# Performance work log

Measured on AMD Instinct MI355X. Metric: run time of the kernel, lower is better.

Reference implementation:

```python
import jax, jax.numpy as jnp
import numpy as np

T, B, D, H, A = 512, 1024, 128, 64, 18


def _mlp(x, W1, b1, W2, b2):
    # two Linear+ReLU layers (MLP with hidden_sizes=(64,64), output_dim=0)
    h = jax.nn.relu(x @ W1.T + b1)
    return jax.nn.relu(h @ W2.T + b2)


def _gru_scan(x, dones, h0, Wih, Whh, bih, bhh):
    # x: [T,B,H], dones: [T,B], h0: [1,B,H]; torch GRU cell with done-reset
    def step(h, inp):
        xt, dt = inp
        h = (1.0 - dt)[:, None] * h  # reset state where episode ended
        gi = xt @ Wih.T + bih        # [B,3H]
        gh = h @ Whh.T + bhh
        ir, iz, i_n = jnp.split(gi, 3, axis=-1)
        hr, hz, h_n = jnp.split(gh, 3, axis=-1)
        r = jax.nn.sigmoid(ir + hr)
        z = jax.nn.sigmoid(iz + hz)
        n = jnp.tanh(i_n + r * h_n)
        h_new = (1.0 - z) * n + z * h
        return h_new, h_new
    hT, hs = jax.lax.scan(step, h0[0], (x, dones))
    return hs, hT[None]  # [T,B,H], [1,B,H]


def setup_inputs() -> dict:
    key = jax.random.key(0)
    ks = jax.random.split(key, 24)
    u = lambda k, shape, fan_in: jax.random.uniform(k, shape, jnp.float32, -1.0, 1.0) / np.sqrt(fan_in)
    inp = {
        'obs': jax.random.normal(ks[0], (T, B, D), jnp.float32),
        'dones': (jax.random.uniform(ks[1], (T, B)) < 0.01).astype(jnp.float32),
        'actor_state': jnp.zeros((1, B, H), jnp.float32),
        'critic_state': jnp.zeros((1, B, H), jnp.float32),
        # actor params
        'aW1': u(ks[2], (H, D), D), 'ab1': u(ks[3], (H,), D),
        'aW2': u(ks[4], (H, H), H), 'ab2': u(ks[5], (H,), H),
        'aWih': u(ks[6], (3 * H, H), H), 'aWhh': u(ks[7], (3 * H, H), H),
        'abih': u(ks[8], (3 * H,), H), 'abhh': u(ks[9], (3 * H,), H),
        'aWl': u(ks[10], (A, H), H), 'abl': u(ks[11], (A,), H),
        # critic params
        'cW1': u(ks[12], (H, D), D), 'cb1': u(ks[13], (H,), D),
        'cW2': u(ks[14], (H, H), H), 'cb2': u(ks[15], (H,), H),
        'cWih': u(ks[16], (3 * H, H), H), 'cWhh': u(ks[17], (3 * H, H), H),
        'cbih': u(ks[18], (3 * H,), H), 'cbhh': u(ks[19], (3 * H,), H),
        'cWv': u(ks[20], (1, H), H), 'cbv': u(ks[21], (1,), H),
    }
    return inp


def reference(obs, dones, actor_state, critic_state,
              aW1, ab1, aW2, ab2, aWih, aWhh, abih, abhh, aWl, abl,
              cW1, cb1, cW2, cb2, cWih, cWhh, cbih, cbhh, cWv, cbv):
    # actor branch
    xa = _mlp(obs, aW1, ab1, aW2, ab2)                              # [T,B,H]
    ha, actor_state = _gru_scan(xa, dones, actor_state, aWih, aWhh, abih, abhh)
    logits = ha @ aWl.T + abl                                       # [T,B,A]
    # critic branch
    xc = _mlp(obs, cW1, cb1, cW2, cb2)
    hc, critic_state = _gru_scan(xc, dones, critic_state, cWih, cWhh, cbih, cbhh)
    values = hc @ cWv.T + cbv                                       # [T,B,1]
    return (logits, values, actor_state, critic_state)
```

## Files before the change

### kernel.cpp

```cpp
#include <hip/hip_runtime.h>
#include <hip/hip_bf16.h>

typedef short short8 __attribute__((ext_vector_type(8)));
typedef float f32x4 __attribute__((ext_vector_type(4)));

#define T_ 512
#define B_ 1024
#define D_ 128
#define H_ 64
#define A_ 18
#define TB_ (T_*B_)

#define XELEMS (TB_*H_)
#define WBASE  (2*XELEMS)
#define WBR    38912
#define W1OFF  0
#define W2OFF  8192
#define WIHOFF 12288
#define WHHOFF 24576
#define WHDOFF 36864

#define LOGN  (TB_*A_)
#define VOFF_ LOGN
#define SOFF_ (LOGN + TB_)

#define S1_ (-1.4426950408889634f)
#define S2_ (-2.885390081777927f)

__device__ __forceinline__ ushort f2bf(float f) {
  __hip_bfloat16 h = __float2bfloat16(f);
  return __builtin_bit_cast(ushort, h);
}
__device__ __forceinline__ uint cvt_pk_bf16(float lo, float hi) {
  uint r;
  asm("v_cvt_pk_bf16_f32 %0, %1, %2" : "=v"(r) : "v"(lo), "v"(hi));
  return r;
}
__device__ __forceinline__ ushort cvt1_bf16(float v) {
  return (ushort)(cvt_pk_bf16(v, v) & 0xffffu);
}
__device__ __forceinline__ f32x4 mfma16(short8 a, short8 b, f32x4 c) {
  return __builtin_amdgcn_mfma_f32_16x16x32_bf16(a, b, c, 0, 0, 0);
}

__global__ __launch_bounds__(256) void prep_kernel(
    const float* aW1, const float* aW2, const float* aWih, const float* aWhh, const float* aWl,
    const float* cW1, const float* cW2, const float* cWih, const float* cWhh, const float* cWv,
    ushort* wts) {
  int idx = blockIdx.x * 256 + threadIdx.x;
  if (idx >= 2*WBR) return;
  int br = idx / WBR, off = idx % WBR;
  float v;
  if      (off < W2OFF)  v = (br ? cW1  : aW1 )[off];
  else if (off < WIHOFF) v = (br ? cW2  : aW2 )[off - W2OFF];
  else if (off < WHHOFF) {
    int rel = off - WIHOFF;
    v = (br ? cWih : aWih)[rel];
    v *= (rel < 128*H_) ? S1_ : S2_;
  }
  else if (off < WHDOFF) {
    int rel = off - WHHOFF;
    v = (br ? cWhh : aWhh)[rel];
    v *= (rel < 128*H_) ? S1_ : S2_;
  }
  else {
    int t = off - WHDOFF;
    if (br == 0) v = (t < A_*H_) ? aWl[t] : 0.f;
    else         v = (t < H_)    ? cWv[t] : 0.f;
  }
  wts[WBASE + idx] = f2bf(v);
}

__global__ __launch_bounds__(256) void mlp_kernel(
    const float* __restrict__ obs, const ushort* __restrict__ wts,
    const float* __restrict__ ab1, const float* __restrict__ ab2,
    const float* __restrict__ cb1, const float* __restrict__ cb2,
    ushort* __restrict__ xout) {
  __shared__ __align__(16) ushort htA[4][16 * H_], htC[4][16 * H_];
  __shared__ __align__(16) ushort wlds[24576];
  const int tid = threadIdx.x;
  const int l = tid & 63, w = tid >> 6;
  const int lr = l & 15, lg = l >> 4;
  const int key = lr & 7;
  const long base = (long)blockIdx.x * 256;
  const ushort* wbA = wts + WBASE;
  const ushort* wbC = wts + WBASE + WBR;

  float b1A[4], b1C[4], b2A[4], b2C[4];
  #pragma unroll
  for (int nt = 0; nt < 4; ++nt) {
    int coln = nt * 16 + lr;
    b1A[nt] = ab1[coln]; b1C[nt] = cb1[coln];
    b2A[nt] = ab2[coln]; b2C[nt] = cb2[coln];
  }

  #pragma unroll
  for (int i = 0; i < 12; ++i) {
    int c = tid + i * 256;
    int seg = (c < 1024) ? 0 : (c < 2048) ? 1 : (c < 2560) ? 2 : 3;
    int cbase = (seg == 0) ? 0 : (seg == 1) ? 1024 : (seg == 2) ? 2048 : 2560;
    int off = (c - cbase) * 8;
    int L = (seg < 2) ? 128 : 64;
    int segdst = (seg == 0) ? 0 : (seg == 1) ? 8192 : (seg == 2) ? 16384 : 20480;
    const ushort* src = (seg == 0) ? wbA + W1OFF + off :
                        (seg == 1) ? wbC + W1OFF + off :
                        (seg == 2) ? wbA + W2OFF + off : wbC + W2OFF + off;
    int n = off / L, ci = (off % L) / 8;
    int cis = (ci & ~7) | ((ci & 7) ^ (n & 7));
    *(uint4*)(wlds + segdst + n * L + cis * 8) = *(const uint4*)src;
  }
  __syncthreads();

  auto getW1 = [&](int br, int n, int ks) -> short8 {
    int ci = ks * 4 + lg;
    int cis = (ci & 8) | ((ci & 7) ^ (n & 7));
    return *(const short8*)(wlds + br * 8192 + n * D_ + cis * 8);
  };
  auto getW2 = [&](int br, int n, int ks) -> short8 {
    int ci = ks * 4 + lg;
    int cis = ci ^ (n & 7);
    return *(const short8*)(wlds + 16384 + br * 4096 + n * H_ + cis * 8);
  };

  auto ldobs = [&](int s, float4 (&buf)[8]) {
    const float* op = obs + (base + s * 64 + (long)w * 16 + lr) * D_;
    #pragma unroll
    for (int ks = 0; ks < 4; ++ks) {
      buf[2 * ks]     = *(const float4*)(op + ks * 32 + lg * 8);
      buf[2 * ks + 1] = *(const float4*)(op + ks * 32 + lg * 8 + 4);
    }
  };

  auto compute = [&](int s, float4 (&buf)[8]) {
    short8 af[4];
    #pragma unroll
    for (int ks = 0; ks < 4; ++ks) {
      uint4 u;
      u.x = cvt_pk_bf16(buf[2 * ks].x, buf[2 * ks].y);
      u.y = cvt_pk_bf16(buf[2 * ks].z, buf[2 * ks].w);
      u.z = cvt_pk_bf16(buf[2 * ks + 1].x, buf[2 * ks + 1].y);
      u.w = cvt_pk_bf16(buf[2 * ks + 1].z, buf[2 * ks + 1].w);
      af[ks] = __builtin_bit_cast(short8, u);
    }
    f32x4 aA[4], aC[4];
    #pragma unroll
    for (int nt = 0; nt < 4; ++nt) {
      aA[nt] = f32x4{b1A[nt], b1A[nt], b1A[nt], b1A[nt]};
      aC[nt] = f32x4{b1C[nt], b1C[nt], b1C[nt], b1C[nt]};
    }
    #pragma unroll
    for (int ks = 0; ks < 4; ++ks) {
      #pragma unroll
      for (int nt = 0; nt < 4; ++nt) {
        int n = nt * 16 + lr;
        aA[nt] = mfma16(af[ks], getW1(0, n, ks), aA[nt]);
        aC[nt] = mfma16(af[ks], getW1(1, n, ks), aC[nt]);
      }
    }
    #pragma unroll
    for (int nt = 0; nt < 4; ++nt) {
      int coln = nt * 16 + lr;
      #pragma unroll
      for (int j = 0; j < 4; ++j) {
        int rw = lg * 4 + j;
        int idx = rw * H_ + ((((coln >> 3) ^ (rw & 7))) << 3) + (coln & 7);
        htA[w][idx] = cvt1_bf16(fmaxf(aA[nt][j], 0.f));
        htC[w][idx] = cvt1_bf16(fmaxf(aC[nt][j], 0.f));
      }
    }
    short8 a2A[2], a2C[2];
    #pragma unroll
    for (int ks = 0; ks < 2; ++ks) {
      int c = ks * 4 + lg;
      a2A[ks] = *(const short8*)(&htA[w][lr * H_ + ((c ^ key) << 3)]);
      a2C[ks] = *(const short8*)(&htC[w][lr * H_ + ((c ^ key) << 3)]);
    }
    f32x4 cA[4], cC[4];
    #pragma unroll
    for (int nt = 0; nt < 4; ++nt) {
      cA[nt] = f32x4{b2A[nt], b2A[nt], b2A[nt], b2A[nt]};
      cC[nt] = f32x4{b2C[nt], b2C[nt], b2C[nt], b2C[nt]};
    }
    #pragma unroll
    for (int ks = 0; ks < 2; ++ks) {
      #pragma unroll
      for (int nt = 0; nt < 4; ++nt) {
        int n = nt * 16 + lr;
        cA[nt] = mfma16(a2A[ks], getW2(0, n, ks), cA[nt]);
        cC[nt] = mfma16(a2C[ks], getW2(1, n, ks), cC[nt]);
      }
    }
    #pragma unroll
    for (int nt = 0; nt < 4; ++nt) {
      int coln = nt * 16 + lr;
      #pragma unroll
      for (int j = 0; j < 4; ++j) {
        int rw = lg * 4 + j;
        int idx = rw * H_ + ((((coln >> 3) ^ (rw & 7))) << 3) + (coln & 7);
        htA[w][idx] = cvt1_bf16(fmaxf(cA[nt][j], 0.f));
        htC[w][idx] = cvt1_bf16(fmaxf(cC[nt][j], 0.f));
      }
    }
    {
      long rt = base + s * 64 + (long)w * 16;
      ushort* dpA = xout + (size_t)rt * H_;
      ushort* dpC = xout + (size_t)XELEMS + (size_t)rt * H_;
      #pragma unroll
      for (int i = 0; i < 2; ++i) {
        int id = l + i * 64;
        int rr = id >> 3, cc = id & 7;
        uint4 vA = *(const uint4*)(&htA[w][rr * H_ + ((cc ^ (rr & 7)) << 3)]);
        *(uint4*)(dpA + rr * H_ + (cc << 3)) = vA;
        uint4 vC = *(const uint4*)(&htC[w][rr * H_ + ((cc ^ (rr & 7)) << 3)]);
        *(uint4*)(dpC + rr * H_ + (cc << 3)) = vC;
      }
    }
  };

  float4 bufA[8], bufB[8];
  ldobs(0, bufA);
  ldobs(1, bufB);
  compute(0, bufA);
  ldobs(2, bufA);
  compute(1, bufB);
  ldobs(3, bufB);
  compute(2, bufA);
  compute(3, bufB);
}

__global__ __launch_bounds__(512, 1) void scan_kernel(
    const ushort* __restrict__ wts,
    const ushort* __restrict__ xin,
    ushort* __restrict__ hist,
    const float* __restrict__ dones,
    const float* __restrict__ astate, const float* __restrict__ cstate,
    const float* __restrict__ abih, const float* __restrict__ abhh,
    const float* __restrict__ cbih, const float* __restrict__ cbhh,
    float* __restrict__ out) {
  __shared__ __align__(16) ushort hbuf[2][16 * H_];
  __shared__ __align__(8)  ushort dl16[T_ * 16];
  __shared__ __align__(16) float  preL[2][3][1024];
  __shared__ __align__(8)  uint2  hhist[2][256];
  const int tid = threadIdx.x;
  const int l = tid & 63, w = tid >> 6;
  const int pw = w & 3;
  const int lr = l & 15, lg = l >> 4;
  const int grp = blockIdx.x & 1;
  const int b0 = (blockIdx.x >> 1) * 16;
  const int slot = pw * 64 + ((l & ~7) | ((l ^ (l >> 3)) & 7));
  const int o4 = pw * 16 + lg * 4;

  const ushort* wb = wts + grp * WBR;
  const ushort* xp = xin + (size_t)grp * XELEMS;
  ushort* hp = hist + (size_t)grp * XELEMS;
  const float* bihp = grp ? cbih : abih;
  const float* bhhp = grp ? cbhh : abhh;
  const float* st   = grp ? cstate : astate;

  #pragma unroll
  for (int i = 0; i < 4; ++i) {
    int s = tid + i * 512;
    int t = s >> 2, p = s & 3;
    float4 v = *(const float4*)(dones + (size_t)t * B_ + b0 + p * 4);
    uint lo = (v.x != 0.f ? 1u : 0u) | ((v.y != 0.f ? 1u : 0u) << 16);
    uint hi = (v.z != 0.f ? 1u : 0u) | ((v.w != 0.f ? 1u : 0u) << 16);
    *(uint2*)(&dl16[t * 16 + p * 4]) = uint2{lo, hi};
  }

  short8 hhW[3][2];
  f32x4 bhnv;
  float h_old[4];
  const int myW = lr * H_ + (((pw * 2 + (lg >> 1)) ^ (lr & 7)) << 3) + (lg & 1) * 4;
  const int rdA = lr * H_ + (((0 + lg) ^ (lr & 7)) << 3);
  const int rdB = lr * H_ + (((4 + lg) ^ (lr & 7)) << 3);

  short8 ihW[3][2];
  f32x4 bs0, bs1, binv;
  short8 pb0[2], pb1[2], pb2[2], pb3[2];

  auto loadx = [&](int t, short8 (&f)[2]) {
    const ushort* p = xp + ((size_t)t * B_ + b0 + lr) * H_;
    f[0] = *(const short8*)(p + lg * 8);
    f[1] = *(const short8*)(p + 32 + lg * 8);
  };
  auto cpre_to = [&](short8 (&xb)[2], int par) {
    f32x4 p0 = bs0, p1 = bs1, p2 = binv;
    p0 = mfma16(ihW[0][0], xb[0], p0); p0 = mfma16(ihW[0][1], xb[1], p0);
    p1 = mfma16(ihW[1][0], xb[0], p1); p1 = mfma16(ihW[1][1], xb[1], p1);
    p2 = mfma16(ihW[2][0], xb[0], p2); p2 = mfma16(ihW[2][1], xb[1], p2);
    *(f32x4*)&preL[par][0][slot * 4] = p0;
    *(f32x4*)&preL[par][1][slot * 4] = p1;
    *(f32x4*)&preL[par][2][slot * 4] = p2;
  };

  if (w < 4) {
    #pragma unroll
    for (int g = 0; g < 3; ++g) {
      int n = g * 64 + pw * 16 + lr;
      #pragma unroll
      for (int ks = 0; ks < 2; ++ks)
        hhW[g][ks] = *(const short8*)(wb + WHHOFF + n * H_ + ks * 32 + lg * 8);
    }
    float4 h2v = *(const float4*)(bhhp + 128 + o4);
    bhnv[0] = S2_ * h2v.x; bhnv[1] = S2_ * h2v.y;
    bhnv[2] = S2_ * h2v.z; bhnv[3] = S2_ * h2v.w;
    float4 h0v = *(const float4*)(st + (size_t)(b0 + lr) * H_ + o4);
    bool rs0 = (dones[b0 + lr] != 0.f);
    h_old[0] = rs0 ? 0.f : h0v.x; h_old[1] = rs0 ? 0.f : h0v.y;
    h_old[2] = rs0 ? 0.f : h0v.z; h_old[3] = rs0 ? 0.f : h0v.w;
    uint2 hv;
    hv.x = cvt_pk_bf16(h_old[0], h_old[1]);
    hv.y = cvt_pk_bf16(h_old[2], h_old[3]);
    *(uint2*)(&hbuf[0][myW]) = hv;
  } else {
    #pragma unroll
    for (int g = 0; g < 3; ++g) {
      int n = g * 64 + pw * 16 + lr;
      #pragma unroll
      for (int ks = 0; ks < 2; ++ks)
        ihW[g][ks] = *(const short8*)(wb + WIHOFF + n * H_ + ks * 32 + lg * 8);
    }
    float4 a0 = *(const float4*)(bihp + o4),       h0v = *(const float4*)(bhhp + o4);
    float4 a1 = *(const float4*)(bihp + 64 + o4),  h1v = *(const float4*)(bhhp + 64 + o4);
    float4 a2 = *(const float4*)(bihp + 128 + o4);
    bs0[0]=S1_*(a0.x+h0v.x); bs0[1]=S1_*(a0.y+h0v.y); bs0[2]=S1_*(a0.z+h0v.z); bs0[3]=S1_*(a0.w+h0v.w);
    bs1[0]=S1_*(a1.x+h1v.x); bs1[1]=S1_*(a1.y+h1v.y); bs1[2]=S1_*(a1.z+h1v.z); bs1[3]=S1_*(a1.w+h1v.w);
    binv[0]=S2_*a2.x; binv[1]=S2_*a2.y; binv[2]=S2_*a2.z; binv[3]=S2_*a2.w;
    loadx(0, pb0);
    cpre_to(pb0, 0);
    loadx(1, pb1); loadx(2, pb2); loadx(3, pb3); loadx(4, pb0);
  }

  __syncthreads();

  if (w < 4) {
    int cur = 0;
    auto cstep = [&](int t) {
      short8 hf0 = *(const short8*)(&hbuf[cur][rdA]);
      short8 hf1 = *(const short8*)(&hbuf[cur][rdB]);
      int par = t & 1;
      f32x4 S0 = *(const f32x4*)&preL[par][0][slot * 4];
      f32x4 S1 = *(const f32x4*)&preL[par][1][slot * 4];
      f32x4 P2 = *(const f32x4*)&preL[par][2][slot * 4];
      f32x4 Gh = bhnv;
      int tn = t + 1;
      ushort dn = dl16[((tn < T_) ? tn : 0) * 16 + lr];
      bool rs = (tn < T_) && (dn != 0);

      S0 = mfma16(hhW[0][0], hf0, S0); S0 = mfma16(hhW[0][1], hf1, S0);
      S1 = mfma16(hhW[1][0], hf0, S1); S1 = mfma16(hhW[1][1], hf1, S1);
      Gh = mfma16(hhW[2][0], hf0, Gh); Gh = mfma16(hhW[2][1], hf1, Gh);

      float hn[4];
      #pragma unroll
      for (int j = 0; j < 4; ++j) {
        float rr = __builtin_amdgcn_rcpf(1.f + __builtin_amdgcn_exp2f(S0[j]));
        float zz = __builtin_amdgcn_rcpf(1.f + __builtin_amdgcn_exp2f(S1[j]));
        float sn = fmaf(rr, Gh[j], P2[j]);
        float qq = __builtin_amdgcn_rcpf(1.f + __builtin_amdgcn_exp2f(sn));
        float nn = fmaf(2.f, qq, -1.f);
        hn[j] = fmaf(zz, h_old[j] - nn, nn);
      }
      uint2 hv;
      hv.x = cvt_pk_bf16(hn[0], hn[1]);
      hv.y = cvt_pk_bf16(hn[2], hn[3]);
      hhist[par][slot] = hv;
      uint2 hz;
      hz.x = rs ? 0u : hv.x;
      hz.y = rs ? 0u : hv.y;
      h_old[0] = rs ? 0.f : hn[0]; h_old[1] = rs ? 0.f : hn[1];
      h_old[2] = rs ? 0.f : hn[2]; h_old[3] = rs ? 0.f : hn[3];
      int nxt = cur ^ 1;
      *(uint2*)(&hbuf[nxt][myW]) = hz;
      asm volatile("s_waitcnt lgkmcnt(0)" ::: "memory");
      __builtin_amdgcn_s_barrier();
      cur = nxt;
    };
    for (int t = 0; t < T_; ++t) cstep(t);
    float4 fs = {h_old[0], h_old[1], h_old[2], h_old[3]};
    *(float4*)(out + SOFF_ + (size_t)grp * (B_ * H_) + (size_t)(b0 + lr) * H_ + o4) = fs;
  } else {
    auto pstep = [&](int t, short8 (&xb)[2]) {
      if (t > 0) {
        uint2 hv2 = hhist[(t - 1) & 1][slot];
        *(uint2*)(hp + ((size_t)(t - 1) * B_ + b0 + lr) * H_ + o4) = hv2;
      }
      if (t + 1 < T_) cpre_to(xb, (t + 1) & 1);
      if (t + 5 < T_) loadx(t + 5, xb);
      asm volatile("s_waitcnt lgkmcnt(0)" ::: "memory");
      __builtin_amdgcn_s_barrier();
    };
    for (int it = 0; it < T_ / 4; ++it) {
      int t = 4 * it;
      pstep(t,     pb1);
      pstep(t + 1, pb2);
      pstep(t + 2, pb3);
      pstep(t + 3, pb0);
    }
    uint2 hv2 = hhist[(T_ - 1) & 1][slot];
    *(uint2*)(hp + ((size_t)(T_ - 1) * B_ + b0 + lr) * H_ + o4) = hv2;
  }
}

__global__ __launch_bounds__(256) void head_kernel(
    const ushort* __restrict__ ws,
    const float* __restrict__ abl, const float* __restrict__ cbv,
    float* __restrict__ out) {
  __shared__ float ltile[4][16 * A_];
  const int tid = threadIdx.x;
  const int l = tid & 63, w = tid >> 6;
  const int lr = l & 15, lg = l >> 4;
  const long r0 = (long)blockIdx.x * 64 + w * 16;
  const f32x4 fzero = {0.f, 0.f, 0.f, 0.f};

  const ushort* hA = ws + r0 * H_;
  const ushort* hC = ws + XELEMS + r0 * H_;
  short8 aA[2], aC[2];
  #pragma unroll
  for (int ks = 0; ks < 2; ++ks) {
    aA[ks] = *(const short8*)(hA + lr * H_ + ks * 32 + lg * 8);
    aC[ks] = *(const short8*)(hC + lr * H_ + ks * 32 + lg * 8);
  }
  const ushort* wbA = ws + WBASE + WHDOFF;
  const ushort* wbC = ws + WBASE + WBR + WHDOFF;
  f32x4 acc[2];
  acc[0] = fzero; acc[1] = fzero;
  #pragma unroll
  for (int nt = 0; nt < 2; ++nt) {
    int n = nt * 16 + lr;
    #pragma unroll
    for (int ks = 0; ks < 2; ++ks) {
      short8 b = *(const short8*)(wbA + n * H_ + ks * 32 + lg * 8);
      acc[nt] = mfma16(aA[ks], b, acc[nt]);
    }
  }
  f32x4 vacc = fzero;
  {
    int n = lr;
    #pragma unroll
    for (int ks = 0; ks < 2; ++ks) {
      short8 b = *(const short8*)(wbC + n * H_ + ks * 32 + lg * 8);
      vacc = mfma16(aC[ks], b, vacc);
    }
  }
  #pragma unroll
  for (int nt = 0; nt < 2; ++nt) {
    int n = nt * 16 + lr;
    if (n < A_) {
      float bias = abl[n];
      #pragma unroll
      for (int j = 0; j < 4; ++j)
        ltile[w][(lg * 4 + j) * A_ + n] = acc[nt][j] + bias;
    }
  }
  asm volatile("s_waitcnt lgkmcnt(0)" ::: "memory");
  #pragma unroll
  for (int i = 0; i < 5; ++i) {
    int idx = l + i * 64;
    if (idx < 16 * A_)
      out[r0 * A_ + idx] = ltile[w][idx];
  }
  if (lr == 0) {
    float bias = cbv[0];
    #pragma unroll
    for (int j = 0; j < 4; ++j)
      out[VOFF_ + r0 + lg * 4 + j] = vacc[j] + bias;
  }
}

extern "C" void kernel_launch(void* const* d_in, const int* in_sizes, int n_in,
                              void* d_out, int out_size, void* d_ws, size_t ws_size,
                              hipStream_t stream) {
  const float* obs    = (const float*)d_in[0];
  const float* dones  = (const float*)d_in[1];
  const float* astate = (const float*)d_in[2];
  const float* cstate = (const float*)d_in[3];
  const float* aW1  = (const float*)d_in[4];
  const float* ab1  = (const float*)d_in[5];
  const float* aW2  = (const float*)d_in[6];
  const float* ab2  = (const float*)d_in[7];
  const float* aWih = (const float*)d_in[8];
  const float* aWhh = (const float*)d_in[9];
  const float* abih = (const float*)d_in[10];
  const float* abhh = (const float*)d_in[11];
  const float* aWl  = (const float*)d_in[12];
  const float* abl  = (const float*)d_in[13];
  const float* cW1  = (const float*)d_in[14];
  const float* cb1  = (const float*)d_in[15];
  const float* cW2  = (const float*)d_in[16];
  const float* cb2  = (const float*)d_in[17];
  const float* cWih = (const float*)d_in[18];
  const float* cWhh = (const float*)d_in[19];
  const float* cbih = (const float*)d_in[20];
  const float* cbhh = (const float*)d_in[21];
  const float* cWv  = (const float*)d_in[22];
  const float* cbv  = (const float*)d_in[23];
  ushort* ws = (ushort*)d_ws;
  float* out = (float*)d_out;

  const size_t need = ((size_t)2 * XELEMS + 2 * WBR) * 2;
  if (ws_size < need) {
    hipMemsetAsync(d_out, 0x7F, 16, stream);
    return;
  }

  hipLaunchKernelGGL(prep_kernel, dim3(304), dim3(256), 0, stream,
                     aW1, aW2, aWih, aWhh, aWl, cW1, cW2, cWih, cWhh, cWv, ws);
  hipLaunchKernelGGL(mlp_kernel, dim3(TB_ / 256), dim3(256), 0, stream,
                     obs, ws, ab1, ab2, cb1, cb2, ws);
  hipLaunchKernelGGL(scan_kernel, dim3(128), dim3(512), 0, stream,
                     ws + WBASE, ws, ws, dones, astate, cstate,
                     abih, abhh, cbih, cbhh, out);
  hipLaunchKernelGGL(head_kernel, dim3(TB_ / 64), dim3(256), 0, stream,
                     ws, abl, cbv, out);
}
```

Before: 329.4 us.

## Fuse output heads into scan producer warps and merge GRU gate reciprocals

The actor/critic output heads (logits and value) are now computed inside the scan kernel's producer warps, straight from the per-step hidden state held in shared memory. This removes the separate head kernel and the write and re-read of the full bf16 hidden-state history in global memory. The GRU cell update is also rewritten algebraically so the z and n gates share one reciprocal instead of three per element. The trade-off is more work on the producer warps, which must stay ahead of the recurrence, and uncoalesced scalar logit stores from inside the scan loop.

After: 337.5 us. 2.4% more time.

```diff
diff --git a/kernel.cpp b/kernel.cpp
--- a/kernel.cpp
+++ b/kernel.cpp
@@ -231,11 +231,11 @@
 __global__ __launch_bounds__(512, 1) void scan_kernel(
     const ushort* __restrict__ wts,
     const ushort* __restrict__ xin,
-    ushort* __restrict__ hist,
     const float* __restrict__ dones,
     const float* __restrict__ astate, const float* __restrict__ cstate,
     const float* __restrict__ abih, const float* __restrict__ abhh,
     const float* __restrict__ cbih, const float* __restrict__ cbhh,
+    const float* __restrict__ abl, const float* __restrict__ cbv,
     float* __restrict__ out) {
   __shared__ __align__(16) ushort hbuf[2][16 * H_];
   __shared__ __align__(8)  ushort dl16[T_ * 16];
@@ -252,7 +252,6 @@
 
   const ushort* wb = wts + grp * WBR;
   const ushort* xp = xin + (size_t)grp * XELEMS;
-  ushort* hp = hist + (size_t)grp * XELEMS;
   const float* bihp = grp ? cbih : abih;
   const float* bhhp = grp ? cbhh : abhh;
   const float* st   = grp ? cstate : astate;
@@ -277,6 +276,8 @@
   short8 ihW[3][2];
   f32x4 bs0, bs1, binv;
   short8 pb0[2], pb1[2], pb2[2], pb3[2];
+  short8 hdA[2][2];
+  f32x4 hbias0, hbias1;
 
   auto loadx = [&](int t, short8 (&f)[2]) {
     const ushort* p = xp + ((size_t)t * B_ + b0 + lr) * H_;
@@ -326,6 +327,22 @@
     bs0[0]=S1_*(a0.x+h0v.x); bs0[1]=S1_*(a0.y+h0v.y); bs0[2]=S1_*(a0.z+h0v.z); bs0[3]=S1_*(a0.w+h0v.w);
     bs1[0]=S1_*(a1.x+h1v.x); bs1[1]=S1_*(a1.y+h1v.y); bs1[2]=S1_*(a1.z+h1v.z); bs1[3]=S1_*(a1.w+h1v.w);
     binv[0]=S2_*a2.x; binv[1]=S2_*a2.y; binv[2]=S2_*a2.z; binv[3]=S2_*a2.w;
+    #pragma unroll
+    for (int tile = 0; tile < 2; ++tile)
+      #pragma unroll
+      for (int ks = 0; ks < 2; ++ks)
+        hdA[tile][ks] = *(const short8*)(wb + WHDOFF + (tile * 16 + lr) * H_ + ks * 32 + lg * 8);
+    #pragma unroll
+    for (int j = 0; j < 4; ++j) {
+      int r0r = lg * 4 + j, r1r = 16 + lg * 4 + j;
+      if (grp == 0) {
+        hbias0[j] = (r0r < A_) ? abl[r0r] : 0.f;
+        hbias1[j] = (r1r < A_) ? abl[r1r] : 0.f;
+      } else {
+        hbias0[j] = (r0r == 0) ? cbv[0] : 0.f;
+        hbias1[j] = 0.f;
+      }
+    }
     loadx(0, pb0);
     cpre_to(pb0, 0);
     loadx(1, pb1); loadx(2, pb2); loadx(3, pb3); loadx(4, pb0);
@@ -354,12 +371,14 @@
       float hn[4];
       #pragma unroll
       for (int j = 0; j < 4; ++j) {
-        float rr = __builtin_amdgcn_rcpf(1.f + __builtin_amdgcn_exp2f(S0[j]));
-        float zz = __builtin_amdgcn_rcpf(1.f + __builtin_amdgcn_exp2f(S1[j]));
+        float Er = __builtin_amdgcn_exp2f(S0[j]);
+        float rr = __builtin_amdgcn_rcpf(1.f + Er);
+        float Ez = __builtin_amdgcn_exp2f(S1[j]);
         float sn = fmaf(rr, Gh[j], P2[j]);
-        float qq = __builtin_amdgcn_rcpf(1.f + __builtin_amdgcn_exp2f(sn));
-        float nn = fmaf(2.f, qq, -1.f);
-        hn[j] = fmaf(zz, h_old[j] - nn, nn);
+        float En = __builtin_amdgcn_exp2f(sn);
+        float num = fmaf(En, h_old[j] - Ez, Ez + h_old[j]);
+        float den = fmaf(En, Ez, 1.f + En + Ez);
+        hn[j] = num * __builtin_amdgcn_rcpf(den);
       }
       uint2 hv;
       hv.x = cvt_pk_bf16(hn[0], hn[1]);
@@ -380,11 +399,47 @@
     float4 fs = {h_old[0], h_old[1], h_old[2], h_old[3]};
     *(float4*)(out + SOFF_ + (size_t)grp * (B_ * H_) + (size_t)(b0 + lr) * H_ + o4) = fs;
   } else {
+    auto headstep = [&](int th) {
+      int par = th & 1;
+      short8 hf[2];
+      #pragma unroll
+      for (int fr = 0; fr < 2; ++fr) {
+        uint2 ua, ub;
+        {
+          int hcol = fr * 32 + lg * 8;
+          int pw_s = hcol >> 4, lg_s = (hcol >> 2) & 3;
+          int l_s = lg_s * 16 + lr;
+          int sl = pw_s * 64 + ((l_s & ~7) | ((l_s ^ (l_s >> 3)) & 7));
+          ua = hhist[par][sl];
+        }
+        {
+          int hcol = fr * 32 + lg * 8 + 4;
+          int pw_s = hcol >> 4, lg_s = (hcol >> 2) & 3;
+          int l_s = lg_s * 16 + lr;
+          int sl = pw_s * 64 + ((l_s & ~7) | ((l_s ^ (l_s >> 3)) & 7));
+          ub = hhist[par][sl];
+        }
+        uint4 q = {ua.x, ua.y, ub.x, ub.y};
+        hf[fr] = __builtin_bit_cast(short8, q);
+      }
+      f32x4 acc0 = hbias0, acc1 = hbias1;
+      acc0 = mfma16(hdA[0][0], hf[0], acc0); acc0 = mfma16(hdA[0][1], hf[1], acc0);
+      acc1 = mfma16(hdA[1][0], hf[0], acc1); acc1 = mfma16(hdA[1][1], hf[1], acc1);
+      size_t rowb = (size_t)th * B_ + b0 + lr;
+      if (grp == 0) {
+        #pragma unroll
+        for (int j = 0; j < 4; ++j) {
+          int r0r = lg * 4 + j;
+          out[rowb * A_ + r0r] = acc0[j];
+          int r1r = 16 + lg * 4 + j;
+          if (r1r < A_) out[rowb * A_ + r1r] = acc1[j];
+        }
+      } else if (lg == 0) {
+        out[VOFF_ + rowb] = acc0[0];
+      }
+    };
     auto pstep = [&](int t, short8 (&xb)[2]) {
-      if (t > 0) {
-        uint2 hv2 = hhist[(t - 1) & 1][slot];
-        *(uint2*)(hp + ((size_t)(t - 1) * B_ + b0 + lr) * H_ + o4) = hv2;
-      }
+      if (t > 0) headstep(t - 1);
       if (t + 1 < T_) cpre_to(xb, (t + 1) & 1);
       if (t + 5 < T_) loadx(t + 5, xb);
       asm volatile("s_waitcnt lgkmcnt(0)" ::: "memory");
@@ -397,74 +452,7 @@
       pstep(t + 2, pb3);
       pstep(t + 3, pb0);
     }
-    uint2 hv2 = hhist[(T_ - 1) & 1][slot];
-    *(uint2*)(hp + ((size_t)(T_ - 1) * B_ + b0 + lr) * H_ + o4) = hv2;
-  }
-}
-
-__global__ __launch_bounds__(256) void head_kernel(
-    const ushort* __restrict__ ws,
-    const float* __restrict__ abl, const float* __restrict__ cbv,
-    float* __restrict__ out) {
-  __shared__ float ltile[4][16 * A_];
-  const int tid = threadIdx.x;
-  const int l = tid & 63, w = tid >> 6;
-  const int lr = l & 15, lg = l >> 4;
-  const long r0 = (long)blockIdx.x * 64 + w * 16;
-  const f32x4 fzero = {0.f, 0.f, 0.f, 0.f};
-
-  const ushort* hA = ws + r0 * H_;
-  const ushort* hC = ws + XELEMS + r0 * H_;
-  short8 aA[2], aC[2];
-  #pragma unroll
-  for (int ks = 0; ks < 2; ++ks) {
-    aA[ks] = *(const short8*)(hA + lr * H_ + ks * 32 + lg * 8);
-    aC[ks] = *(const short8*)(hC + lr * H_ + ks * 32 + lg * 8);
-  }
-  const ushort* wbA = ws + WBASE + WHDOFF;
-  const ushort* wbC = ws + WBASE + WBR + WHDOFF;
-  f32x4 acc[2];
-  acc[0] = fzero; acc[1] = fzero;
-  #pragma unroll
-  for (int nt = 0; nt < 2; ++nt) {
-    int n = nt * 16 + lr;
-    #pragma unroll
-    for (int ks = 0; ks < 2; ++ks) {
-      short8 b = *(const short8*)(wbA + n * H_ + ks * 32 + lg * 8);
-      acc[nt] = mfma16(aA[ks], b, acc[nt]);
-    }
-  }
-  f32x4 vacc = fzero;
-  {
-    int n = lr;
-    #pragma unroll
-    for (int ks = 0; ks < 2; ++ks) {
-      short8 b = *(const short8*)(wbC + n * H_ + ks * 32 + lg * 8);
-      vacc = mfma16(aC[ks], b, vacc);
-    }
-  }
-  #pragma unroll
-  for (int nt = 0; nt < 2; ++nt) {
-    int n = nt * 16 + lr;
-    if (n < A_) {
-      float bias = abl[n];
-      #pragma unroll
-      for (int j = 0; j < 4; ++j)
-        ltile[w][(lg * 4 + j) * A_ + n] = acc[nt][j] + bias;
-    }
-  }
-  asm volatile("s_waitcnt lgkmcnt(0)" ::: "memory");
-  #pragma unroll
-  for (int i = 0; i < 5; ++i) {
-    int idx = l + i * 64;
-    if (idx < 16 * A_)
-      out[r0 * A_ + idx] = ltile[w][idx];
-  }
-  if (lr == 0) {
-    float bias = cbv[0];
-    #pragma unroll
-    for (int j = 0; j < 4; ++j)
-      out[VOFF_ + r0 + lg * 4 + j] = vacc[j] + bias;
+    headstep(T_ - 1);
   }
 }
 
@@ -509,8 +497,6 @@
   hipLaunchKernelGGL(mlp_kernel, dim3(TB_ / 256), dim3(256), 0, stream,
                      obs, ws, ab1, ab2, cb1, cb2, ws);
   hipLaunchKernelGGL(scan_kernel, dim3(128), dim3(512), 0, stream,
-                     ws + WBASE, ws, ws, dones, astate, cstate,
-                     abih, abhh, cbih, cbhh, out);
-  hipLaunchKernelGGL(head_kernel, dim3(TB_ / 64), dim3(256), 0, stream,
-                     ws, abl, cbv, out);
-}
+                     ws + WBASE, ws, dones, astate, cstate,
+                     abih, abhh, cbih, cbhh, abl, cbv, out);
+}
```
